# Performance work log

Hardware: AMD Instinct MI355X
Metric: run time of the kernel (lower is better)

The kernel has to match this reference:

```python
import jax, jax.numpy as jnp
import numpy as np

N, E, HID, STRUCT = 50000, 800000, 128, 7
GAMMA, DELTA = 1.0, 0.5
LN_EPS = 1e-5


def seg_softmax(score, seg, num_segments):
    m = jax.ops.segment_max(score, seg, num_segments=num_segments)
    e = jnp.exp(score - m[seg])
    s = jax.ops.segment_sum(e, seg, num_segments=num_segments)
    return e / s[seg]


def setup_inputs() -> dict:
    key = jax.random.key(0)
    ks = jax.random.split(key, 16)
    w = lambda k, shp: (jax.random.normal(k, shp, dtype=jnp.float32) * 0.1)
    return {
        "edge_index": jax.random.randint(ks[0], (2, E), 0, N, dtype=jnp.int32),
        "h": jax.random.normal(ks[1], (N, HID), dtype=jnp.float32),
        "W_att": w(ks[2], (HID, HID)),
        "phi_att_w": w(ks[3], (HID, HID)),
        "phi_att_b": jnp.zeros((HID,), jnp.float32),
        "W_p": w(ks[4], (HID, HID)),
        "W_p_prime": w(ks[5], (HID, HID)),
        "f_def_w": w(ks[6], (HID, 1)),
        "f_def_b": jnp.zeros((1,), jnp.float32),
        "W_self_w": w(ks[7], (HID, HID)),
        "W_self_b": jnp.zeros((HID,), jnp.float32),
        "W_A_w": w(ks[8], (HID, HID)),
        "W_A_b": jnp.zeros((HID,), jnp.float32),
        "W_str_w": w(ks[9], (STRUCT - 1, HID)),
        "W_str_b": jnp.zeros((HID,), jnp.float32),
        "ln_g": jnp.ones((HID,), jnp.float32),
        "ln_b": jnp.zeros((HID,), jnp.float32),
    }


def reference(edge_index, h, W_att, phi_att_w, phi_att_b, W_p, W_p_prime,
              f_def_w, f_def_b, W_self_w, W_self_b, W_A_w, W_A_b,
              W_str_w, W_str_b, ln_g, ln_b):
    H = h  # in_dim == hidden_dim -> embed is None
    s_feat = h[:, : STRUCT - 1]                       # [N, 6]
    src, tgt = edge_index[0], edge_index[1]
    h_src, h_tgt = H[src], H[tgt]                     # [E, HID]
    s_src, s_tgt = s_feat[src], s_feat[tgt]           # [E, 6]

    # attention scores, scatter-softmax over tgt
    W_hs = h_src @ W_att
    score = jnp.sum(h_tgt * W_hs, -1) + jnp.sum(s_src * s_tgt, -1)
    alpha = seg_softmax(score, tgt, N)                # [E]

    # defense term on reversed edges: rev_src = tgt, rev_tgt = src
    h_att, h_def = H[src], H[tgt]                     # H[rev_tgt], H[rev_src]
    pair = jnp.sum((h_att @ W_p) * (h_def @ W_p_prime), -1)
    beta = seg_softmax(pair, src, N)                  # softmax over rev_tgt = src
    psi = (h_def @ f_def_w + f_def_b)[:, 0]           # [E]
    sum_term = jax.ops.segment_sum(beta * jnp.exp(-psi), src, num_segments=N)
    d = -jnp.log(sum_term + 1e-8)
    rho = jax.nn.sigmoid(GAMMA * (d - DELTA))         # [N]

    rho_edge = rho[src]
    m_e = alpha[:, None] * (h_src @ phi_att_w + phi_att_b) * (1.0 - rho_edge)[:, None]
    m_att = jax.ops.segment_sum(m_e, tgt, num_segments=N)  # [N, HID]

    H_new = jax.nn.relu(H @ W_self_w + W_self_b + m_att @ W_A_w + W_A_b
                        + s_feat @ W_str_w + W_str_b) + H
    mu = jnp.mean(H_new, -1, keepdims=True)
    var = jnp.mean((H_new - mu) ** 2, -1, keepdims=True)
    return (H_new - mu) * jax.lax.rsqrt(var + LN_EPS) * ln_g + ln_b
```

## Files before the change

### kernel.cpp

```cpp
#include <hip/hip_runtime.h>
#include <math.h>

#define HID 128
#define NSTR 6
#define GAMMA 1.0f
#define DELTA 0.5f
#define LN_EPS 1e-5f
#define KPAD 72
#define CSR_CHUNK 8192

typedef __attribute__((ext_vector_type(4))) float f4;
typedef __attribute__((ext_vector_type(8))) short bf16x8;
typedef __attribute__((ext_vector_type(4))) float f32x4;

__device__ __forceinline__ unsigned short f2bf(float f) {
    unsigned u = __float_as_uint(f);
    unsigned r = u + 0x7FFFu + ((u >> 16) & 1u);
    return (unsigned short)(r >> 16);
}
__device__ __forceinline__ float bf2f(unsigned short h) {
    return __uint_as_float((unsigned)h << 16);
}
__device__ __forceinline__ void split2(float v, unsigned short& h, unsigned short& l) {
    h = f2bf(v);
    l = f2bf(v - bf2f(h));
}
__device__ __forceinline__ void bf2f2(unsigned u, float& lo, float& hi) {
    lo = __uint_as_float(u << 16);
    hi = __uint_as_float(u & 0xFFFF0000u);
}
__device__ __forceinline__ void unpack8(const uint4 u, float* f) {
    bf2f2(u.x, f[0], f[1]); bf2f2(u.y, f[2], f[3]);
    bf2f2(u.z, f[4], f[5]); bf2f2(u.w, f[6], f[7]);
}

__global__ __launch_bounds__(256) void k_prep_all(
    const float* __restrict__ W_att, const float* __restrict__ Wself,
    const float* __restrict__ Wp,    const float* __restrict__ Wpp,
    const float* __restrict__ phiw,  const float* __restrict__ WA,
    const float* __restrict__ phib,
    unsigned short* __restrict__ WT, float* __restrict__ pbA)
{
    __shared__ float Bs[128][129];
    __shared__ float As[16][129];
    const int mode = blockIdx.y, c0 = blockIdx.x * 16;
    const int tid = threadIdx.x;
    const size_t MSZ = (size_t)2 * HID * HID;
    unsigned short* hi = WT + (size_t)mode * MSZ;
    unsigned short* lo = hi + HID * HID;

    if (mode == 0) {
        for (int idx = tid; idx < 2048; idx += 256) {
            const int c = idx >> 7, k = idx & 127;
            unsigned short h, l;
            split2(W_att[(size_t)(c0 + c) * HID + k], h, l);
            hi[(size_t)(c0 + c) * HID + k] = h;
            lo[(size_t)(c0 + c) * HID + k] = l;
        }
    } else if (mode == 1) {
        for (int idx = tid; idx < 2048; idx += 256) {
            const int k = idx >> 4, c = idx & 15;
            Bs[k][c] = Wself[k * HID + c0 + c];
        }
        __syncthreads();
        for (int idx = tid; idx < 2048; idx += 256) {
            const int c = idx >> 7, k = idx & 127;
            unsigned short h, l;
            split2(Bs[k][c], h, l);
            hi[(size_t)(c0 + c) * HID + k] = h;
            lo[(size_t)(c0 + c) * HID + k] = l;
        }
    } else if (mode == 2) {
        for (int idx = tid; idx < 128 * 128; idx += 256)
            Bs[idx >> 7][idx & 127] = Wpp[idx];
        for (int idx = tid; idx < 16 * 128; idx += 256)
            As[idx >> 7][idx & 127] = Wp[(size_t)(c0 + (idx >> 7)) * HID + (idx & 127)];
        __syncthreads();
        for (int it = 0; it < 8; ++it) {
            const int idx = tid + 256 * it;
            const int c = idx >> 7, k = idx & 127;
            float a = 0.f;
            #pragma unroll 4
            for (int j = 0; j < 128; ++j)
                a = fmaf(As[c][j], Bs[k][j], a);
            unsigned short h, l;
            split2(a, h, l);
            hi[(size_t)(c0 + c) * HID + k] = h;
            lo[(size_t)(c0 + c) * HID + k] = l;
        }
    } else {
        for (int idx = tid; idx < 128 * 128; idx += 256)
            Bs[idx >> 7][idx & 127] = phiw[idx];
        for (int idx = tid; idx < 16 * 128; idx += 256) {
            const int c = idx >> 7, j = idx & 127;
            As[c][j] = WA[(size_t)j * HID + c0 + c];
        }
        __syncthreads();
        for (int it = 0; it < 8; ++it) {
            const int idx = tid + 256 * it;
            const int c = idx >> 7, k = idx & 127;
            float a = 0.f;
            #pragma unroll 4
            for (int j = 0; j < 128; ++j)
                a = fmaf(As[c][j], Bs[k][j], a);
            unsigned short h, l;
            split2(a, h, l);
            hi[(size_t)(c0 + c) * HID + k] = h;
            lo[(size_t)(c0 + c) * HID + k] = l;
        }
        if (tid < 16) {
            float a = 0.f;
            #pragma unroll 4
            for (int j = 0; j < 128; ++j)
                a = fmaf(phib[j], As[tid][j], a);
            pbA[c0 + tid] = a;
        }
    }
}

__global__ __launch_bounds__(256) void k_cast_count(
    const float* __restrict__ H, const float* __restrict__ fw,
    const float* __restrict__ fb,
    unsigned short* __restrict__ HB, float* __restrict__ psi,
    const int* __restrict__ etgt, const int* __restrict__ esrc,
    int* __restrict__ cnt_t, int* __restrict__ cnt_s,
    int nbCast, int NB, int NC, int E, int N)
{
    __shared__ int cnt[256];
    const int tid = threadIdx.x;
    const int bid = blockIdx.x;
    if (bid < nbCast) {
        const int row = bid * 16 + (tid >> 4), sub = tid & 15;
        if (row >= N) return;
        const size_t o = (size_t)row * HID + sub * 8;
        const f4 v0 = *(const f4*)&H[o];
        const f4 v1 = *(const f4*)&H[o + 4];
        ushort4 a, b;
        a.x = f2bf(v0[0]); a.y = f2bf(v0[1]); a.z = f2bf(v0[2]); a.w = f2bf(v0[3]);
        b.x = f2bf(v1[0]); b.y = f2bf(v1[1]); b.z = f2bf(v1[2]); b.w = f2bf(v1[3]);
        *(ushort4*)&HB[o] = a;
        *(ushort4*)&HB[o + 4] = b;
        const f4 w0 = *(const f4*)&fw[sub * 8];
        const f4 w1 = *(const f4*)&fw[sub * 8 + 4];
        float s = v0[0]*w0[0] + v0[1]*w0[1] + v0[2]*w0[2] + v0[3]*w0[3]
                + v1[0]*w1[0] + v1[1]*w1[1] + v1[2]*w1[2] + v1[3]*w1[3];
        #pragma unroll
        for (int mk = 1; mk < 16; mk <<= 1) s += __shfl_xor(s, mk);
        if (sub == 0) psi[row] = s + fb[0];
    } else {
        const int rem = bid - nbCast;
        const int which = rem / NC, blk = rem % NC;
        const int* __restrict__ key = which ? esrc : etgt;
        int* __restrict__ outc = which ? cnt_s : cnt_t;
        for (int i = tid; i < NB; i += 256) cnt[i] = 0;
        __syncthreads();
        const int e0 = blk * CSR_CHUNK;
        const int e1 = min(e0 + CSR_CHUNK, E);
        for (int e = e0 + tid; e < e1; e += 256)
            atomicAdd(&cnt[key[e] >> 8], 1);
        __syncthreads();
        for (int k = tid; k < NB; k += 256)
            outc[(size_t)k * NC + blk] = cnt[k];
    }
}

struct GemmArgsT {
    const unsigned short* Whi[2];
    const unsigned short* Wlo[2];
    void*                 O[2];
    int                   of32[2];
};

__global__ __launch_bounds__(256, 2) void k_gemm(const float* __restrict__ A,
                                                 GemmArgsT g, int N)
{
    extern __shared__ unsigned short lds[];
    unsigned short* Ahi = lds;
    unsigned short* Alo = lds + 128 * KPAD;
    unsigned short* Bhi = lds + 2 * 128 * KPAD;
    unsigned short* Blo = lds + 3 * 128 * KPAD;
    const int tid  = threadIdx.x;
    const int row0 = blockIdx.x * 128;
    const int nrows = min(128, N - row0);
    const int ph   = blockIdx.y;
    const int w    = tid >> 6, lane = tid & 63;
    const int lrow = lane & 15, kgrp = lane >> 4;

    f32x4 acc[2][8];
    #pragma unroll
    for (int tc = 0; tc < 8; ++tc) {
        acc[0][tc] = f32x4{0.f, 0.f, 0.f, 0.f};
        acc[1][tc] = f32x4{0.f, 0.f, 0.f, 0.f};
    }

    const unsigned short* __restrict__ Wh = g.Whi[ph];
    const unsigned short* __restrict__ Wl = g.Wlo[ph];

    for (int ch = 0; ch < 2; ++ch) {
        __syncthreads();
        #pragma unroll
        for (int it = 0; it < 8; ++it) {
            const int idx = tid + 256 * it;
            const int r = idx >> 4, kq = (idx & 15) * 4;
            f4 v = {0.f, 0.f, 0.f, 0.f};
            if (r < nrows) v = *(const f4*)&A[(size_t)(row0 + r) * HID + ch * 64 + kq];
            ushort4 h, l;
            split2(v[0], h.x, l.x); split2(v[1], h.y, l.y);
            split2(v[2], h.z, l.z); split2(v[3], h.w, l.w);
            *(ushort4*)&Ahi[r * KPAD + kq] = h;
            *(ushort4*)&Alo[r * KPAD + kq] = l;
        }
        #pragma unroll
        for (int it = 0; it < 4; ++it) {
            const int idx = tid + 256 * it;
            const int c = idx >> 3, k8 = (idx & 7) * 8;
            *(uint4*)&Bhi[c * KPAD + k8] = *(const uint4*)&Wh[(size_t)c * HID + ch * 64 + k8];
            *(uint4*)&Blo[c * KPAD + k8] = *(const uint4*)&Wl[(size_t)c * HID + ch * 64 + k8];
        }
        __syncthreads();

        #pragma unroll
        for (int ks = 0; ks < 2; ++ks) {
            const int ko = ks * 32 + kgrp * 8;
            bf16x8 ah[2], al[2], bh[8], bl[8];
            #pragma unroll
            for (int tr = 0; tr < 2; ++tr) {
                const int rr = w * 32 + tr * 16 + lrow;
                ah[tr] = *(const bf16x8*)&Ahi[rr * KPAD + ko];
                al[tr] = *(const bf16x8*)&Alo[rr * KPAD + ko];
            }
            #pragma unroll
            for (int tc = 0; tc < 8; ++tc) {
                const int cc = tc * 16 + lrow;
                bh[tc] = *(const bf16x8*)&Bhi[cc * KPAD + ko];
                bl[tc] = *(const bf16x8*)&Blo[cc * KPAD + ko];
            }
            #pragma unroll
            for (int tr = 0; tr < 2; ++tr)
                #pragma unroll
                for (int tc = 0; tc < 8; ++tc) {
                    acc[tr][tc] = __builtin_amdgcn_mfma_f32_16x16x32_bf16(ah[tr], bh[tc], acc[tr][tc], 0, 0, 0);
                    acc[tr][tc] = __builtin_amdgcn_mfma_f32_16x16x32_bf16(al[tr], bh[tc], acc[tr][tc], 0, 0, 0);
                    acc[tr][tc] = __builtin_amdgcn_mfma_f32_16x16x32_bf16(ah[tr], bl[tc], acc[tr][tc], 0, 0, 0);
                }
        }
    }

    #pragma unroll
    for (int tr = 0; tr < 2; ++tr)
        #pragma unroll
        for (int j = 0; j < 4; ++j) {
            const int r = w * 32 + tr * 16 + kgrp * 4 + j;
            if (r < nrows) {
                if (g.of32[ph]) {
                    float* O = (float*)g.O[ph];
                    #pragma unroll
                    for (int tc = 0; tc < 8; ++tc)
                        O[(size_t)(row0 + r) * HID + tc * 16 + lrow] = acc[tr][tc][j];
                } else {
                    unsigned short* O = (unsigned short*)g.O[ph];
                    #pragma unroll
                    for (int tc = 0; tc < 8; ++tc)
                        O[(size_t)(row0 + r) * HID + tc * 16 + lrow] = f2bf(acc[tr][tc][j]);
                }
            }
        }
}

__global__ __launch_bounds__(256, 2) void k_final(
    const float* __restrict__ Agg, const float* __restrict__ H,
    const float* __restrict__ sig, const float* __restrict__ pbA,
    const unsigned short* __restrict__ Ghi, const unsigned short* __restrict__ Glo,
    const unsigned short* __restrict__ WShi, const unsigned short* __restrict__ WSlo,
    const float* __restrict__ Wstr,
    const float* __restrict__ bself, const float* __restrict__ bA,
    const float* __restrict__ bstr,
    const float* __restrict__ lng, const float* __restrict__ lnb,
    float* __restrict__ out, int N)
{
    extern __shared__ unsigned short lds[];
    unsigned short* Ahi = lds;
    unsigned short* Alo = lds + 128 * KPAD;
    unsigned short* Bhi = lds + 2 * 128 * KPAD;
    unsigned short* Blo = lds + 3 * 128 * KPAD;
    const int tid  = threadIdx.x;
    const int row0 = blockIdx.x * 128;
    const int nrows = min(128, N - row0);
    const int w    = tid >> 6, lane = tid & 63;
    const int lrow = lane & 15, kgrp = lane >> 4;

    f32x4 acc[2][8];
    float gl[8], bl_[8], pb[8];
    #pragma unroll
    for (int tc = 0; tc < 8; ++tc) {
        const int c = tc * 16 + lrow;
        const float bv = bself[c] + bA[c] + bstr[c];
        acc[0][tc] = f32x4{bv, bv, bv, bv};
        acc[1][tc] = f32x4{bv, bv, bv, bv};
        gl[tc] = lng[c]; bl_[tc] = lnb[c]; pb[tc] = pbA[c];
    }

    for (int ph = 0; ph < 2; ++ph) {
        const float* __restrict__ Am = ph ? H : Agg;
        const unsigned short* __restrict__ Wh = ph ? WShi : Ghi;
        const unsigned short* __restrict__ Wl = ph ? WSlo : Glo;
        for (int ch = 0; ch < 2; ++ch) {
            __syncthreads();
            #pragma unroll
            for (int it = 0; it < 8; ++it) {
                const int idx = tid + 256 * it;
                const int r = idx >> 4, kq = (idx & 15) * 4;
                f4 v = {0.f, 0.f, 0.f, 0.f};
                if (r < nrows) v = *(const f4*)&Am[(size_t)(row0 + r) * HID + ch * 64 + kq];
                ushort4 h, l;
                split2(v[0], h.x, l.x); split2(v[1], h.y, l.y);
                split2(v[2], h.z, l.z); split2(v[3], h.w, l.w);
                *(ushort4*)&Ahi[r * KPAD + kq] = h;
                *(ushort4*)&Alo[r * KPAD + kq] = l;
            }
            #pragma unroll
            for (int it = 0; it < 4; ++it) {
                const int idx = tid + 256 * it;
                const int c = idx >> 3, k8 = (idx & 7) * 8;
                *(uint4*)&Bhi[c * KPAD + k8] = *(const uint4*)&Wh[(size_t)c * HID + ch * 64 + k8];
                *(uint4*)&Blo[c * KPAD + k8] = *(const uint4*)&Wl[(size_t)c * HID + ch * 64 + k8];
            }
            __syncthreads();

            #pragma unroll
            for (int ks = 0; ks < 2; ++ks) {
                const int ko = ks * 32 + kgrp * 8;
                bf16x8 ah[2], al[2], bh[8], bl[8];
                #pragma unroll
                for (int tr = 0; tr < 2; ++tr) {
                    const int rr = w * 32 + tr * 16 + lrow;
                    ah[tr] = *(const bf16x8*)&Ahi[rr * KPAD + ko];
                    al[tr] = *(const bf16x8*)&Alo[rr * KPAD + ko];
                }
                #pragma unroll
                for (int tc = 0; tc < 8; ++tc) {
                    const int cc = tc * 16 + lrow;
                    bh[tc] = *(const bf16x8*)&Bhi[cc * KPAD + ko];
                    bl[tc] = *(const bf16x8*)&Blo[cc * KPAD + ko];
                }
                #pragma unroll
                for (int tr = 0; tr < 2; ++tr)
                    #pragma unroll
                    for (int tc = 0; tc < 8; ++tc) {
                        acc[tr][tc] = __builtin_amdgcn_mfma_f32_16x16x32_bf16(ah[tr], bh[tc], acc[tr][tc], 0, 0, 0);
                        acc[tr][tc] = __builtin_amdgcn_mfma_f32_16x16x32_bf16(al[tr], bh[tc], acc[tr][tc], 0, 0, 0);
                        acc[tr][tc] = __builtin_amdgcn_mfma_f32_16x16x32_bf16(ah[tr], bl[tc], acc[tr][tc], 0, 0, 0);
                    }
            }

            if (ph == 1 && ch == 0) {
                #pragma unroll
                for (int tr = 0; tr < 2; ++tr)
                    #pragma unroll
                    for (int j = 0; j < 4; ++j) {
                        const int rr = w * 32 + tr * 16 + kgrp * 4 + j;
                        float s[NSTR];
                        #pragma unroll
                        for (int k = 0; k < NSTR; ++k)
                            s[k] = bf2f(Ahi[rr * KPAD + k]) + bf2f(Alo[rr * KPAD + k]);
                        #pragma unroll
                        for (int tc = 0; tc < 8; ++tc) {
                            float a = 0.f;
                            #pragma unroll
                            for (int k = 0; k < NSTR; ++k)
                                a = fmaf(s[k], Wstr[k * HID + tc * 16 + lrow], a);
                            acc[tr][tc][j] += a;
                        }
                    }
            }
        }
    }

    #pragma unroll
    for (int tr = 0; tr < 2; ++tr)
        #pragma unroll
        for (int j = 0; j < 4; ++j) {
            const int r = w * 32 + tr * 16 + kgrp * 4 + j;
            const bool valid = r < nrows;
            const size_t rb = (size_t)(row0 + r) * HID;
            const float sg = valid ? sig[row0 + r] : 0.f;
            float v[8], s1 = 0.f, s2 = 0.f;
            #pragma unroll
            for (int tc = 0; tc < 8; ++tc) {
                float x = fmaxf(acc[tr][tc][j] + sg * pb[tc], 0.f);
                if (valid) x += H[rb + tc * 16 + lrow];
                v[tc] = x;
                s1 += x; s2 += x * x;
            }
            #pragma unroll
            for (int mk = 1; mk < 16; mk <<= 1) {
                s1 += __shfl_xor(s1, mk);
                s2 += __shfl_xor(s2, mk);
            }
            const float mean = s1 * (1.f / HID);
            const float var  = s2 * (1.f / HID) - mean * mean;
            const float rs   = rsqrtf(var + LN_EPS);
            if (valid) {
                #pragma unroll
                for (int tc = 0; tc < 8; ++tc)
                    out[rb + tc * 16 + lrow] = (v[tc] - mean) * rs * gl[tc] + bl_[tc];
            }
        }
}

__global__ __launch_bounds__(1024) void k_csr_scan(
    const int* __restrict__ cnt_t, int* __restrict__ off_t,
    const int* __restrict__ cnt_s, int* __restrict__ off_s, int L)
{
    const int* __restrict__ cnt = blockIdx.x ? cnt_s : cnt_t;
    int* __restrict__ off = blockIdx.x ? off_s : off_t;
    __shared__ int warp_sums[16];
    __shared__ int carry_s;
    const int tid = threadIdx.x, lane = tid & 63, wid = tid >> 6;
    if (tid == 0) carry_s = 0;
    __syncthreads();
    for (int i0 = 0; i0 < L; i0 += 1024) {
        const int i = i0 + tid;
        const int v = (i < L) ? cnt[i] : 0;
        int x = v;
        #pragma unroll
        for (int d = 1; d < 64; d <<= 1) {
            const int y = __shfl_up(x, d);
            if (lane >= d) x += y;
        }
        if (lane == 63) warp_sums[wid] = x;
        __syncthreads();
        if (wid == 0) {
            int ws = (lane < 16) ? warp_sums[lane] : 0;
            #pragma unroll
            for (int d = 1; d < 16; d <<= 1) {
                const int y = __shfl_up(ws, d);
                if (lane >= d) ws += y;
            }
            if (lane < 16) warp_sums[lane] = ws;
        }
        __syncthreads();
        const int carry = carry_s;
        if (i < L) off[i] = carry + (wid ? warp_sums[wid - 1] : 0) + x - v;
        __syncthreads();
        if (tid == 1023) carry_s = carry + warp_sums[15];
        __syncthreads();
    }
    if (tid == 0) off[L] = carry_s;
}

__global__ __launch_bounds__(256) void k_csr_bucket(
    const int* __restrict__ etgt, const int* __restrict__ esrc,
    const int* __restrict__ off_t, const int* __restrict__ off_s,
    int2* __restrict__ ebuck_t, int2* __restrict__ ebuck_s,
    int NB, int NC, int E)
{
    __shared__ int cur[256];
    const int which = blockIdx.y;
    const int* __restrict__ key = which ? esrc : etgt;
    const int* __restrict__ oth = which ? etgt : esrc;
    const int* __restrict__ off = which ? off_s : off_t;
    int2* __restrict__ ebuck = which ? ebuck_s : ebuck_t;
    const int tid = threadIdx.x;
    for (int k = tid; k < NB; k += 256)
        cur[k] = off[(size_t)k * NC + blockIdx.x];
    __syncthreads();
    const int e0 = blockIdx.x * CSR_CHUNK;
    const int e1 = min(e0 + CSR_CHUNK, E);
    for (int e = e0 + tid; e < e1; e += 256) {
        const int kk = key[e];
        const int p = atomicAdd(&cur[kk >> 8], 1);
        ebuck[p] = make_int2(e, (oth[e] << 8) | (kk & 255));
    }
}

__global__ __launch_bounds__(256) void k_csr_final(
    const int* __restrict__ off_t, const int* __restrict__ off_s,
    const int2* __restrict__ ebuck_t, const int2* __restrict__ ebuck_s,
    int* __restrict__ base_t, int* __restrict__ base_s,
    int* __restrict__ eid_t, int* __restrict__ eid_s,
    int* __restrict__ src_t, int* __restrict__ tgt_s,
    int NB, int NC, int N, int E)
{
    __shared__ int cnt[256], excl[256], wsum[4];
    const int which = blockIdx.y;
    const int* __restrict__ off   = which ? off_s : off_t;
    const int2* __restrict__ ebuck = which ? ebuck_s : ebuck_t;
    int* __restrict__ base = which ? base_s : base_t;
    int* __restrict__ eid  = which ? eid_s : eid_t;
    int* __restrict__ aux  = which ? tgt_s : src_t;
    const int tid = threadIdx.x, lane = tid & 63, wv = tid >> 6;
    const int k = blockIdx.x;
    const int segb = off[(size_t)k * NC];
    const int sege = (k + 1 < NB) ? off[(size_t)(k + 1) * NC] : E;
    cnt[tid] = 0;
    __syncthreads();
    for (int i = segb + tid; i < sege; i += 256)
        atomicAdd(&cnt[ebuck[i].y & 255], 1);
    __syncthreads();
    {
        const int orig = cnt[tid];
        int x = orig;
        #pragma unroll
        for (int d = 1; d < 64; d <<= 1) {
            const int y = __shfl_up(x, d);
            if (lane >= d) x += y;
        }
        if (lane == 63) wsum[wv] = x;
        __syncthreads();
        if (tid == 0) {
            int a = 0;
            #pragma unroll
            for (int i = 0; i < 4; ++i) { const int t = wsum[i]; wsum[i] = a; a += t; }
        }
        __syncthreads();
        excl[tid] = x - orig + wsum[wv];
    }
    __syncthreads();
    const int node = k * 256 + tid;
    if (node < N) base[node] = segb + excl[tid];
    if (k == NB - 1 && tid == 0) base[N] = E;
    cnt[tid] = excl[tid];
    __syncthreads();
    for (int i = segb + tid; i < sege; i += 256) {
        const int2 p = ebuck[i];
        const int r = atomicAdd(&cnt[p.y & 255], 1);
        eid[segb + r] = p.x;
        aux[segb + r] = p.y >> 8;
    }
}

__global__ __launch_bounds__(256) void k_score(
    const int* __restrict__ eid_t, const int* __restrict__ base_t,
    const int* __restrict__ src_t,
    const float* __restrict__ Wt, const unsigned short* __restrict__ UB,
    const unsigned short* __restrict__ HB,
    float* __restrict__ score, float* __restrict__ pairv,
    float* __restrict__ sumt_inv, int N)
{
    const int lane = threadIdx.x & 63, wv = threadIdx.x >> 6;
    const int t = blockIdx.x * 4 + wv;
    if (t >= N) return;
    const int b0 = base_t[t], deg = base_t[t + 1] - b0;
    if (deg == 0) { if (lane == 0) sumt_inv[t] = 0.f; return; }
    const int sub = lane & 15, grp = lane >> 4;
    const size_t to = (size_t)t * HID;

    float wt[8], u[8], htg[8];
    {
        const f4 w0 = *(const f4*)&Wt[to + sub * 8];
        const f4 w1 = *(const f4*)&Wt[to + sub * 8 + 4];
        wt[0] = w0[0]; wt[1] = w0[1]; wt[2] = w0[2]; wt[3] = w0[3];
        wt[4] = w1[0]; wt[5] = w1[1]; wt[6] = w1[2]; wt[7] = w1[3];
        unpack8(*(const uint4*)&UB[to + sub * 8], u);
        unpack8(*(const uint4*)&HB[to + sub * 8], htg);
    }

    bool valN = grp < deg;
    int eidN = 0, srcN = 0;
    if (valN) { eidN = eid_t[b0 + grp]; srcN = src_t[b0 + grp]; }

    for (int j0 = 0; j0 < deg; j0 += 4) {
        const bool val = valN;
        const int eid = eidN, src = srcN;
        const uint4 raw = *(const uint4*)&HB[(size_t)src * HID + sub * 8];
        const int jn = j0 + 4 + grp;
        valN = jn < deg;
        eidN = 0; srcN = 0;
        if (valN) { eidN = eid_t[b0 + jn]; srcN = src_t[b0 + jn]; }

        float hs[8];
        unpack8(raw, hs);
        float ps = 0.f, pp = 0.f;
        #pragma unroll
        for (int d = 0; d < 8; ++d) {
            ps = fmaf(wt[d], hs[d], ps);
            pp = fmaf(u[d], hs[d], pp);
        }
        if (sub == 0) {
            #pragma unroll
            for (int d = 0; d < NSTR; ++d) ps = fmaf(htg[d], hs[d], ps);
        }
        #pragma unroll
        for (int mk = 1; mk < 16; mk <<= 1) {
            ps += __shfl_xor(ps, mk);
            pp += __shfl_xor(pp, mk);
        }
        if (sub == 0 && val) {
            score[b0 + j0 + grp] = ps;
            pairv[eid] = pp;
        }
    }

    float m = -1e30f;
    for (int i = lane; i < deg; i += 64) m = fmaxf(m, score[b0 + i]);
    #pragma unroll
    for (int mk = 1; mk < 64; mk <<= 1) m = fmaxf(m, __shfl_xor(m, mk));
    float psum = 0.f;
    for (int i = lane; i < deg; i += 64) {
        const float e = expf(score[b0 + i] - m);
        score[b0 + i] = e;
        psum += e;
    }
    #pragma unroll
    for (int mk = 1; mk < 64; mk <<= 1) psum += __shfl_xor(psum, mk);
    if (lane == 0) sumt_inv[t] = 1.f / psum;
}

__global__ __launch_bounds__(256) void k_beta2(
    const int* __restrict__ base_s, const int* __restrict__ eid_s,
    const int* __restrict__ tgt_s,
    const float* __restrict__ pairv, const float* __restrict__ psi,
    float* __restrict__ rho1m, int N)
{
    const int lane = threadIdx.x & 63, wv = threadIdx.x >> 6;
    const int s = blockIdx.x * 4 + wv;
    if (s >= N) return;
    const int b0 = base_s[s], deg = base_s[s + 1] - b0;

    float se = 0.f, sn = 0.f;
    if (deg <= 64) {
        const bool v = lane < deg;
        float pv = -1e30f;
        int tg = 0;
        if (v) { pv = pairv[eid_s[b0 + lane]]; tg = tgt_s[b0 + lane]; }
        float m = pv;
        #pragma unroll
        for (int mk = 1; mk < 64; mk <<= 1) m = fmaxf(m, __shfl_xor(m, mk));
        const float ex = v ? expf(pv - m) : 0.f;
        se = ex;
        sn = v ? ex * expf(-psi[tg]) : 0.f;
    } else {
        float m = -1e30f;
        for (int i = lane; i < deg; i += 64) m = fmaxf(m, pairv[eid_s[b0 + i]]);
        #pragma unroll
        for (int mk = 1; mk < 64; mk <<= 1) m = fmaxf(m, __shfl_xor(m, mk));
        for (int i = lane; i < deg; i += 64) {
            const float ex = expf(pairv[eid_s[b0 + i]] - m);
            se += ex;
            sn += ex * expf(-psi[tgt_s[b0 + i]]);
        }
    }
    #pragma unroll
    for (int mk = 1; mk < 64; mk <<= 1) {
        se += __shfl_xor(se, mk);
        sn += __shfl_xor(sn, mk);
    }
    if (lane == 0) {
        const float st = (deg > 0 && se > 0.f) ? sn / se : 0.f;
        const float d  = -logf(st + 1e-8f);
        rho1m[s] = 1.f - 1.f / (1.f + expf(-(GAMMA * (d - DELTA))));
    }
}

__global__ __launch_bounds__(256) void k_matt(
    const int* __restrict__ src_t, const int* __restrict__ base_t,
    const float* __restrict__ score, const float* __restrict__ sumt_inv,
    const float* __restrict__ rho1m,
    const unsigned short* __restrict__ HB,
    float* __restrict__ agg, float* __restrict__ sig, int N)
{
    const int lane = threadIdx.x & 63, wv = threadIdx.x >> 6;
    const int t = blockIdx.x * 4 + wv;
    if (t >= N) return;
    const int b0 = base_t[t], deg = base_t[t + 1] - b0;
    const int sub = lane & 15, grp = lane >> 4;
    const size_t to = (size_t)t * HID;

    float acc[8];
    #pragma unroll
    for (int d = 0; d < 8; ++d) acc[d] = 0.f;
    float csum = 0.f;
    const float inv = (deg > 0) ? sumt_inv[t] : 0.f;

    bool vA = grp < deg, vB = 4 + grp < deg;
    int sA = 0, sB = 0;
    float scA = 0.f, scB = 0.f;
    if (vA) { sA = src_t[b0 + grp];     scA = score[b0 + grp]; }
    if (vB) { sB = src_t[b0 + 4 + grp]; scB = score[b0 + 4 + grp]; }

    for (int j0 = 0; j0 < deg; j0 += 8) {
        const bool cvA = vA, cvB = vB;
        const int csA = sA, csB = sB;
        const float cscA = scA, cscB = scB;
        const float rhoA = cvA ? rho1m[csA] : 0.f;
        const float rhoB = cvB ? rho1m[csB] : 0.f;
        const uint4 rA = *(const uint4*)&HB[(size_t)csA * HID + sub * 8];
        const uint4 rB = *(const uint4*)&HB[(size_t)csB * HID + sub * 8];
        const int jA = j0 + 8 + grp, jB = j0 + 12 + grp;
        vA = jA < deg; vB = jB < deg;
        sA = sB = 0; scA = scB = 0.f;
        if (vA) { sA = src_t[b0 + jA]; scA = score[b0 + jA]; }
        if (vB) { sB = src_t[b0 + jB]; scB = score[b0 + jB]; }

        const float cA = cvA ? cscA * inv * rhoA : 0.f;
        const float cB = cvB ? cscB * inv * rhoB : 0.f;
        float hA[8], hB[8];
        unpack8(rA, hA); unpack8(rB, hB);
        #pragma unroll
        for (int d = 0; d < 8; ++d) {
            acc[d] = fmaf(cA, hA[d], acc[d]);
            acc[d] = fmaf(cB, hB[d], acc[d]);
        }
        if (sub == 0) csum += cA + cB;
    }
    #pragma unroll
    for (int d = 0; d < 8; ++d) {
        acc[d] += __shfl_xor(acc[d], 16);
        acc[d] += __shfl_xor(acc[d], 32);
    }
    csum += __shfl_xor(csum, 16);
    csum += __shfl_xor(csum, 32);
    if (grp == 0) {
        f4 o0, o1;
        #pragma unroll
        for (int d = 0; d < 4; ++d) { o0[d] = acc[d]; o1[d] = acc[d + 4]; }
        *(f4*)&agg[to + sub * 8]     = o0;
        *(f4*)&agg[to + sub * 8 + 4] = o1;
        if (sub == 0) sig[t] = csum;
    }
}

extern "C" void kernel_launch(void* const* d_in, const int* in_sizes, int n_in,
                              void* d_out, int out_size, void* d_ws, size_t ws_size,
                              hipStream_t stream)
{
    const int*   eidx   = (const int*)  d_in[0];
    const float* H      = (const float*)d_in[1];
    const float* W_att  = (const float*)d_in[2];
    const float* phi_w  = (const float*)d_in[3];
    const float* phi_b  = (const float*)d_in[4];
    const float* W_p    = (const float*)d_in[5];
    const float* W_pp   = (const float*)d_in[6];
    const float* fdef_w = (const float*)d_in[7];
    const float* fdef_b = (const float*)d_in[8];
    const float* Wself  = (const float*)d_in[9];
    const float* bself  = (const float*)d_in[10];
    const float* WA     = (const float*)d_in[11];
    const float* bA     = (const float*)d_in[12];
    const float* Wstr   = (const float*)d_in[13];
    const float* bstr   = (const float*)d_in[14];
    const float* lng    = (const float*)d_in[15];
    const float* lnb    = (const float*)d_in[16];
    float* out = (float*)d_out;

    const int E = in_sizes[0] / 2;
    const int N = in_sizes[1] / HID;
    const int* esrc = eidx;
    const int* etgt = eidx + E;

    const int NB = (N + 255) >> 8;
    const int NC = (E + CSR_CHUNK - 1) / CSR_CHUNK;
    const int L  = NB * NC;

    char* w = (char*)d_ws;
    const size_t NHb  = (size_t)N * HID * sizeof(unsigned short);
    const size_t NH   = (size_t)N * HID * sizeof(float);
    const size_t Epad = (((size_t)E * sizeof(float)) + 255) & ~255ull;
    const size_t Npad = (((size_t)(N + 1) * sizeof(float)) + 255) & ~255ull;
    const size_t Lpad = (((size_t)(L + 1) * sizeof(int)) + 255) & ~255ull;

    float*          Wt    = (float*)w;          w += NH;
    unsigned short* UB    = (unsigned short*)w; w += NHb;
    unsigned short* HB    = (unsigned short*)w; w += NHb;
    float* score   = (float*)w; w += Epad;
    float* pairv   = (float*)w; w += Epad;
    int*   eid_t   = (int*)  w; w += Epad;
    int*   eid_s   = (int*)  w; w += Epad;
    int*   src_t   = (int*)  w; w += Epad;
    int*   tgt_s   = (int*)  w; w += Epad;
    int2*  ebuck_t = (int2*) w; w += 2 * Epad;
    int2*  ebuck_s = (int2*) w; w += 2 * Epad;
    int*   cnt_t = (int*)w; w += Lpad;
    int*   off_t = (int*)w; w += Lpad;
    int*   cnt_s = (int*)w; w += Lpad;
    int*   off_s = (int*)w; w += Lpad;
    int*   base_t   = (int*)  w; w += Npad;
    int*   base_s   = (int*)  w; w += Npad;
    float* sumt_inv = (float*)w; w += Npad;
    float* psi      = (float*)w; w += Npad;
    float* rho1m    = (float*)w; w += Npad;
    float* sig      = (float*)w; w += Npad;
    float* pbA      = (float*)w; w += 512;
    unsigned short* WT = (unsigned short*)w;
    w += 4 * 2 * HID * HID * sizeof(unsigned short);
    float* agg = Wt;

    const int nblk128 = (N + 127) / 128;
    const int nblkN4  = (N + 3) / 4;
    const int nbCast  = (N + 15) / 16;
    const size_t lds_mfma = 4 * 128 * KPAD * sizeof(unsigned short);
    const size_t MSZ = (size_t)2 * HID * HID;

    k_prep_all<<<dim3(8, 4), 256, 0, stream>>>(W_att, Wself, W_p, W_pp,
                                               phi_w, WA, phi_b, WT, pbA);

    k_cast_count<<<nbCast + 2 * NC, 256, 0, stream>>>(H, fdef_w, fdef_b, HB, psi,
                                                      etgt, esrc, cnt_t, cnt_s,
                                                      nbCast, NB, NC, E, N);

    GemmArgsT g2;
    g2.Whi[0] = WT;           g2.Wlo[0] = WT + HID * HID;
    g2.Whi[1] = WT + 2 * MSZ; g2.Wlo[1] = WT + 2 * MSZ + HID * HID;
    g2.O[0] = Wt;  g2.of32[0] = 1;
    g2.O[1] = UB;  g2.of32[1] = 0;
    k_gemm<<<dim3(nblk128, 2), 256, lds_mfma, stream>>>(H, g2, N);

    k_csr_scan<<<2, 1024, 0, stream>>>(cnt_t, off_t, cnt_s, off_s, L);
    k_csr_bucket<<<dim3(NC, 2), 256, 0, stream>>>(etgt, esrc, off_t, off_s,
                                                  ebuck_t, ebuck_s, NB, NC, E);
    k_csr_final<<<dim3(NB, 2), 256, 0, stream>>>(off_t, off_s,
                                                 ebuck_t, ebuck_s, base_t, base_s,
                                                 eid_t, eid_s, src_t, tgt_s,
                                                 NB, NC, N, E);

    k_score<<<nblkN4, 256, 0, stream>>>(eid_t, base_t, src_t, Wt, UB, HB,
                                        score, pairv, sumt_inv, N);
    k_beta2<<<nblkN4, 256, 0, stream>>>(base_s, eid_s, tgt_s, pairv, psi, rho1m, N);

    k_matt<<<nblkN4, 256, 0, stream>>>(src_t, base_t, score, sumt_inv,
                                       rho1m, HB, agg, sig, N);

    k_final<<<nblk128, 256, lds_mfma, stream>>>(agg, H, sig, pbA,
                                                WT + 3 * MSZ, WT + 3 * MSZ + HID * HID,
                                                WT + 1 * MSZ, WT + 1 * MSZ + HID * HID,
                                                Wstr, bself, bA, bstr, lng, lnb, out, N);
}
```

Baseline: 273.4 us.

## Precompute bf16 hi/lo splits of H and aggregate once for GEMM kernels

Adds a k_splitlo kernel that writes the bf16 low residual of H into the freed ebuck_t buffer, reusing the existing HB as the high part. k_gemm and k_final now load pre-split hi/lo bf16 tiles instead of re-reading fp32 and splitting per block. k_matt emits the aggregate as hi/lo bf16 directly. The GEMM launch moves after the CSR build so ebuck_t can be reused. The aim is to cut the split ALU work and keep the same byte count per tile, at the cost of an extra kernel pass over H and more buffer aliasing.

```diff
diff --git a/kernel.cpp b/kernel.cpp
--- a/kernel.cpp
+++ b/kernel.cpp
@@ -164,6 +164,24 @@
     }
 }
 
+__global__ __launch_bounds__(256) void k_splitlo(
+    const float* __restrict__ H, unsigned short* __restrict__ HBlo, int total8)
+{
+    const int idx = blockIdx.x * 256 + threadIdx.x;
+    if (idx >= total8) return;
+    const size_t o = (size_t)idx * 8;
+    const f4 v0 = *(const f4*)&H[o];
+    const f4 v1 = *(const f4*)&H[o + 4];
+    ushort4 a, b;
+    unsigned short h;
+    split2(v0[0], h, a.x); split2(v0[1], h, a.y);
+    split2(v0[2], h, a.z); split2(v0[3], h, a.w);
+    split2(v1[0], h, b.x); split2(v1[1], h, b.y);
+    split2(v1[2], h, b.z); split2(v1[3], h, b.w);
+    *(ushort4*)&HBlo[o] = a;
+    *(ushort4*)&HBlo[o + 4] = b;
+}
+
 struct GemmArgsT {
     const unsigned short* Whi[2];
     const unsigned short* Wlo[2];
@@ -171,8 +189,9 @@
     int                   of32[2];
 };
 
-__global__ __launch_bounds__(256, 2) void k_gemm(const float* __restrict__ A,
-                                                 GemmArgsT g, int N)
+__global__ __launch_bounds__(256, 2) void k_gemm(
+    const unsigned short* __restrict__ Ah, const unsigned short* __restrict__ Al,
+    GemmArgsT g, int N)
 {
     extern __shared__ unsigned short lds[];
     unsigned short* Ahi = lds;
@@ -199,16 +218,17 @@
     for (int ch = 0; ch < 2; ++ch) {
         __syncthreads();
         #pragma unroll
-        for (int it = 0; it < 8; ++it) {
+        for (int it = 0; it < 4; ++it) {
             const int idx = tid + 256 * it;
-            const int r = idx >> 4, kq = (idx & 15) * 4;
-            f4 v = {0.f, 0.f, 0.f, 0.f};
-            if (r < nrows) v = *(const f4*)&A[(size_t)(row0 + r) * HID + ch * 64 + kq];
-            ushort4 h, l;
-            split2(v[0], h.x, l.x); split2(v[1], h.y, l.y);
-            split2(v[2], h.z, l.z); split2(v[3], h.w, l.w);
-            *(ushort4*)&Ahi[r * KPAD + kq] = h;
-            *(ushort4*)&Alo[r * KPAD + kq] = l;
+            const int r = idx >> 3, k8 = (idx & 7) * 8;
+            uint4 h = {0u,0u,0u,0u}, l = {0u,0u,0u,0u};
+            if (r < nrows) {
+                const size_t go = (size_t)(row0 + r) * HID + ch * 64 + k8;
+                h = *(const uint4*)&Ah[go];
+                l = *(const uint4*)&Al[go];
+            }
+            *(uint4*)&Ahi[r * KPAD + k8] = h;
+            *(uint4*)&Alo[r * KPAD + k8] = l;
         }
         #pragma unroll
         for (int it = 0; it < 4; ++it) {
@@ -268,7 +288,9 @@
 }
 
 __global__ __launch_bounds__(256, 2) void k_final(
-    const float* __restrict__ Agg, const float* __restrict__ H,
+    const unsigned short* __restrict__ AggHi, const unsigned short* __restrict__ AggLo,
+    const unsigned short* __restrict__ Hhi, const unsigned short* __restrict__ Hlo,
+    const float* __restrict__ H,
     const float* __restrict__ sig, const float* __restrict__ pbA,
     const unsigned short* __restrict__ Ghi, const unsigned short* __restrict__ Glo,
     const unsigned short* __restrict__ WShi, const unsigned short* __restrict__ WSlo,
@@ -301,22 +323,24 @@
     }
 
     for (int ph = 0; ph < 2; ++ph) {
-        const float* __restrict__ Am = ph ? H : Agg;
+        const unsigned short* __restrict__ Amh = ph ? Hhi : AggHi;
+        const unsigned short* __restrict__ Aml = ph ? Hlo : AggLo;
         const unsigned short* __restrict__ Wh = ph ? WShi : Ghi;
         const unsigned short* __restrict__ Wl = ph ? WSlo : Glo;
         for (int ch = 0; ch < 2; ++ch) {
             __syncthreads();
             #pragma unroll
-            for (int it = 0; it < 8; ++it) {
+            for (int it = 0; it < 4; ++it) {
                 const int idx = tid + 256 * it;
-                const int r = idx >> 4, kq = (idx & 15) * 4;
-                f4 v = {0.f, 0.f, 0.f, 0.f};
-                if (r < nrows) v = *(const f4*)&Am[(size_t)(row0 + r) * HID + ch * 64 + kq];
-                ushort4 h, l;
-                split2(v[0], h.x, l.x); split2(v[1], h.y, l.y);
-                split2(v[2], h.z, l.z); split2(v[3], h.w, l.w);
-                *(ushort4*)&Ahi[r * KPAD + kq] = h;
-                *(ushort4*)&Alo[r * KPAD + kq] = l;
+                const int r = idx >> 3, k8 = (idx & 7) * 8;
+                uint4 h = {0u,0u,0u,0u}, l = {0u,0u,0u,0u};
+                if (r < nrows) {
+                    const size_t go = (size_t)(row0 + r) * HID + ch * 64 + k8;
+                    h = *(const uint4*)&Amh[go];
+                    l = *(const uint4*)&Aml[go];
+                }
+                *(uint4*)&Ahi[r * KPAD + k8] = h;
+                *(uint4*)&Alo[r * KPAD + k8] = l;
             }
             #pragma unroll
             for (int it = 0; it < 4; ++it) {
@@ -658,7 +682,8 @@
     const float* __restrict__ score, const float* __restrict__ sumt_inv,
     const float* __restrict__ rho1m,
     const unsigned short* __restrict__ HB,
-    float* __restrict__ agg, float* __restrict__ sig, int N)
+    unsigned short* __restrict__ aggHi, unsigned short* __restrict__ aggLo,
+    float* __restrict__ sig, int N)
 {
     const int lane = threadIdx.x & 63, wv = threadIdx.x >> 6;
     const int t = blockIdx.x * 4 + wv;
@@ -712,11 +737,15 @@
     csum += __shfl_xor(csum, 16);
     csum += __shfl_xor(csum, 32);
     if (grp == 0) {
-        f4 o0, o1;
-        #pragma unroll
-        for (int d = 0; d < 4; ++d) { o0[d] = acc[d]; o1[d] = acc[d + 4]; }
-        *(f4*)&agg[to + sub * 8]     = o0;
-        *(f4*)&agg[to + sub * 8 + 4] = o1;
+        ushort4 h0, h1, l0, l1;
+        split2(acc[0], h0.x, l0.x); split2(acc[1], h0.y, l0.y);
+        split2(acc[2], h0.z, l0.z); split2(acc[3], h0.w, l0.w);
+        split2(acc[4], h1.x, l1.x); split2(acc[5], h1.y, l1.y);
+        split2(acc[6], h1.z, l1.z); split2(acc[7], h1.w, l1.w);
+        *(ushort4*)&aggHi[to + sub * 8]     = h0;
+        *(ushort4*)&aggHi[to + sub * 8 + 4] = h1;
+        *(ushort4*)&aggLo[to + sub * 8]     = l0;
+        *(ushort4*)&aggLo[to + sub * 8 + 4] = l1;
         if (sub == 0) sig[t] = csum;
     }
 }
@@ -784,7 +813,9 @@
     float* pbA      = (float*)w; w += 512;
     unsigned short* WT = (unsigned short*)w;
     w += 4 * 2 * HID * HID * sizeof(unsigned short);
-    float* agg = Wt;
+    unsigned short* HBlo  = (unsigned short*)ebuck_t;
+    unsigned short* aggHi = (unsigned short*)Wt;
+    unsigned short* aggLo = aggHi + (size_t)N * HID;
 
     const int nblk128 = (N + 127) / 128;
     const int nblkN4  = (N + 3) / 4;
@@ -798,13 +829,6 @@
     k_cast_count<<<nbCast + 2 * NC, 256, 0, stream>>>(H, fdef_w, fdef_b, HB, psi,
                                                       etgt, esrc, cnt_t, cnt_s,
                                                       nbCast, NB, NC, E, N);
-
-    GemmArgsT g2;
-    g2.Whi[0] = WT;           g2.Wlo[0] = WT + HID * HID;
-    g2.Whi[1] = WT + 2 * MSZ; g2.Wlo[1] = WT + 2 * MSZ + HID * HID;
-    g2.O[0] = Wt;  g2.of32[0] = 1;
-    g2.O[1] = UB;  g2.of32[1] = 0;
-    k_gemm<<<dim3(nblk128, 2), 256, lds_mfma, stream>>>(H, g2, N);
 
     k_csr_scan<<<2, 1024, 0, stream>>>(cnt_t, off_t, cnt_s, off_s, L);
     k_csr_bucket<<<dim3(NC, 2), 256, 0, stream>>>(etgt, esrc, off_t, off_s,
@@ -814,14 +838,24 @@
                                                  eid_t, eid_s, src_t, tgt_s,
                                                  NB, NC, N, E);
 
+    k_splitlo<<<(N * HID / 8 + 255) / 256, 256, 0, stream>>>(H, HBlo, N * HID / 8);
+
+    GemmArgsT g2;
+    g2.Whi[0] = WT;           g2.Wlo[0] = WT + HID * HID;
+    g2.Whi[1] = WT + 2 * MSZ; g2.Wlo[1] = WT + 2 * MSZ + HID * HID;
+    g2.O[0] = Wt;  g2.of32[0] = 1;
+    g2.O[1] = UB;  g2.of32[1] = 0;
+    k_gemm<<<dim3(nblk128, 2), 256, lds_mfma, stream>>>(HB, HBlo, g2, N);
+
     k_score<<<nblkN4, 256, 0, stream>>>(eid_t, base_t, src_t, Wt, UB, HB,
                                         score, pairv, sumt_inv, N);
     k_beta2<<<nblkN4, 256, 0, stream>>>(base_s, eid_s, tgt_s, pairv, psi, rho1m, N);
 
     k_matt<<<nblkN4, 256, 0, stream>>>(src_t, base_t, score, sumt_inv,
-                                       rho1m, HB, agg, sig, N);
-
-    k_final<<<nblk128, 256, lds_mfma, stream>>>(agg, H, sig, pbA,
+                                       rho1m, HB, aggHi, aggLo, sig, N);
+
+    k_final<<<nblk128, 256, lds_mfma, stream>>>(aggHi, aggLo, HB, HBlo, H,
+                                                sig, pbA,
                                                 WT + 3 * MSZ, WT + 3 * MSZ + HID * HID,
                                                 WT + 1 * MSZ, WT + 1 * MSZ + HID * HID,
                                                 Wstr, bself, bA, bstr, lng, lnb, out, N);
```

New measurement: 273.4 us. About the same (-0.0%).
